# Performance work log

Hardware: AMD Instinct MI355X
Metric: run time of the kernel (lower is better)

## Reference

```python
import jax, jax.numpy as jnp
import numpy as np
import math

B, S, D, DFF = 32, 2048, 512, 512


def setup_inputs() -> dict:
    key = jax.random.key(0)
    ks = jax.random.split(key, 10)
    s = 1.0 / math.sqrt(D)
    inp = {
        "x": jax.random.normal(ks[0], (B, S, D), dtype=jnp.float32),
        "Wq": jax.random.uniform(ks[1], (DFF, D), jnp.float32, -s, s),
        "bq": jax.random.uniform(ks[2], (DFF,), jnp.float32, -s, s),
        "Wk": jax.random.uniform(ks[3], (DFF, D), jnp.float32, -s, s),
        "bk": jax.random.uniform(ks[4], (DFF,), jnp.float32, -s, s),
        "Wv": jax.random.uniform(ks[5], (DFF, D), jnp.float32, -s, s),
        "bv": jax.random.uniform(ks[6], (DFF,), jnp.float32, -s, s),
        "Wt": jax.random.uniform(ks[7], (1, S), jnp.float32, -1.0 / math.sqrt(S), 1.0 / math.sqrt(S)),
        "bt": jax.random.uniform(ks[8], (1,), jnp.float32, -1.0 / math.sqrt(S), 1.0 / math.sqrt(S)),
    }
    return inp


def reference(x, Wq, bq, Wk, bk, Wv, bv, Wt, bt):
    # QKV projections: [B,S,DFF]
    q = jnp.einsum('bsd,fd->bsf', x, Wq) + bq
    k = jnp.einsum('bsd,fd->bsf', x, Wk) + bk
    v = jnp.einsum('bsd,fd->bsf', x, Wv) + bv
    # attention scores: [B,S,S]
    scores = jnp.einsum('bsf,btf->bst', q, k) / math.sqrt(DFF)
    # temporal reduction Linear(S->1): [B,S,1] -> [B,S]
    ta = jnp.einsum('bst,t->bs', scores, Wt[0]) + bt[0]
    # V-weighted sum: [B,DFF]
    latent = jnp.einsum('bsf,bs->bf', v, ta)
    return latent
```

## Files before the change

kernel.cpp:

```cpp
#include <hip/hip_runtime.h>

#define NB 32
#define NS 2048
#define ND 512
#define NFF 512
#define SCALE 0.044194173824159216f
#define CPB 32
#define ROWS 64

__device__ __forceinline__ float dot4(float4 a, float4 b) {
    return a.x * b.x + a.y * b.y + a.z * b.z + a.w * b.w;
}

__device__ __forceinline__ float wave_reduce(float p) {
#pragma unroll
    for (int m = 1; m < 64; m <<= 1) p += __shfl_xor(p, m, 64);
    return p;
}

__global__ void __launch_bounds__(256) k_xw(const float* __restrict__ x,
                                            const float* __restrict__ Wt,
                                            float* __restrict__ xwp) {
    const int b = blockIdx.x >> 5;
    const int chunk = blockIdx.x & 31;
    const int s0 = chunk * ROWS;
    const int t = threadIdx.x;
    const int col = t & 127;
    const int half = t >> 7;

    const float4* xb = (const float4*)(x + (size_t)b * NS * ND);
    float4 acc = make_float4(0.f, 0.f, 0.f, 0.f);
#pragma unroll 8
    for (int i = 0; i < 32; i++) {
        int s = s0 + half + 2 * i;
        float w = Wt[s];
        float4 v = xb[(size_t)s * 128 + col];
        acc.x += w * v.x; acc.y += w * v.y; acc.z += w * v.z; acc.w += w * v.w;
    }
    __shared__ float4 red[128];
    if (half == 1) red[col] = acc;
    __syncthreads();
    if (half == 0) {
        float4 o = red[col];
        o.x += acc.x; o.y += acc.y; o.z += acc.z; o.w += acc.w;
        ((float4*)xwp)[(size_t)blockIdx.x * 128 + col] = o;
    }
}

__global__ void __launch_bounds__(1024, 1)
k_mid(const float* __restrict__ xwp, const float* __restrict__ Wt,
      const float* __restrict__ Wk, const float* __restrict__ bk,
      const float* __restrict__ Wq, const float* __restrict__ bq,
      const float* __restrict__ bt, float* __restrict__ wqs,
      float* __restrict__ cb2) {
    const int b = blockIdx.x;
    const int t = threadIdx.x;
    const int c4 = t & 127;
    const int grp = t >> 7;
    __shared__ __align__(16) float4 tmp4[1024];
    __shared__ __align__(16) float sxw[ND];
    __shared__ float skw[NFF];
    __shared__ float sW[16];
    __shared__ float ssw;

    {
        const float4* xp = (const float4*)(xwp + (size_t)b * CPB * ND) + c4;
        float4 a = make_float4(0.f, 0.f, 0.f, 0.f);
#pragma unroll
        for (int c = 0; c < 4; c++) {
            float4 v = xp[(size_t)(grp * 4 + c) * 128];
            a.x += v.x; a.y += v.y; a.z += v.z; a.w += v.w;
        }
        tmp4[t] = a;
    }
    if (t < 64) {
        float s = 0.f;
#pragma unroll
        for (int i = 0; i < 32; i++) s += Wt[t + 64 * i];
        s = wave_reduce(s);
        if (t == 0) ssw = s;
    }
    __syncthreads();
    if (t < 128) {
        float4 a = tmp4[t];
#pragma unroll
        for (int g = 1; g < 8; g++) {
            float4 v = tmp4[g * 128 + t];
            a.x += v.x; a.y += v.y; a.z += v.z; a.w += v.w;
        }
        ((float4*)sxw)[t] = a;
    }
    __syncthreads();

    const int wv = t >> 6;
    const int lane = t & 63;
    const float sw = ssw;
    const float4 xa = ((const float4*)sxw)[lane];
    const float4 xc = ((const float4*)sxw)[64 + lane];
    float cbp = 0.f;
#pragma unroll
    for (int j = 0; j < 4; j++) {
        const int f = wv * 32 + j * 8;
        float p[8];
#pragma unroll
        for (int u = 0; u < 8; u++) {
            const float4* r = (const float4*)(Wk + (size_t)(f + u) * ND);
            p[u] = dot4(xa, r[lane]) + dot4(xc, r[64 + lane]);
        }
#pragma unroll
        for (int m = 1; m < 64; m <<= 1) {
#pragma unroll
            for (int u = 0; u < 8; u++) p[u] += __shfl_xor(p[u], m, 64);
        }
        if (lane == 0) {
#pragma unroll
            for (int u = 0; u < 8; u++) {
                float k = SCALE * (p[u] + bk[f + u] * sw);
                skw[f + u] = k;
                cbp += k * bq[f + u];
            }
        }
    }
    if (lane == 0) sW[wv] = cbp;
    __syncthreads();

    {
        float4 acc = make_float4(0.f, 0.f, 0.f, 0.f);
        const float4* wq4 = (const float4*)Wq + c4;
#pragma unroll 4
        for (int j = 0; j < 64; j++) {
            int f = grp * 64 + j;
            float kf = skw[f];
            float4 v = wq4[(size_t)f * 128];
            acc.x += kf * v.x; acc.y += kf * v.y;
            acc.z += kf * v.z; acc.w += kf * v.w;
        }
        tmp4[t] = acc;
    }
    __syncthreads();
    if (t < 128) {
        float4 a = tmp4[t];
#pragma unroll
        for (int g = 1; g < 8; g++) {
            float4 v = tmp4[g * 128 + t];
            a.x += v.x; a.y += v.y; a.z += v.z; a.w += v.w;
        }
        ((float4*)(wqs + b * ND))[t] = a;
    }
    if (t == 0) {
        float cb = 0.f;
#pragma unroll
        for (int i = 0; i < 16; i++) cb += sW[i];
        cb2[b] = cb + bt[0];
    }
}

__global__ void __launch_bounds__(256) k_ta_xt(const float* __restrict__ x,
                                               const float* __restrict__ wqs,
                                               const float* __restrict__ cb2,
                                               float* __restrict__ xtp,
                                               float* __restrict__ stp) {
    const int b = blockIdx.x >> 5;
    const int chunk = blockIdx.x & 31;
    const int wv = threadIdx.x >> 6;
    const int lane = threadIdx.x & 63;
    const float4* xb = (const float4*)(x + (size_t)b * NS * ND);
    const float4* wq4 = (const float4*)(wqs + b * ND);
    const float4 w0 = wq4[lane];
    const float4 w1 = wq4[64 + lane];
    const float c = cb2[b];

    float4 a0 = make_float4(0.f, 0.f, 0.f, 0.f);
    float4 a1 = make_float4(0.f, 0.f, 0.f, 0.f);
    float sta = 0.f;
#pragma unroll
    for (int pass = 0; pass < 2; pass++) {
        const int sbase = chunk * ROWS + wv * 16 + pass * 8;
        float4 v0[8], v1[8];
        float pd[8];
#pragma unroll
        for (int i = 0; i < 8; i++) {
            int s = sbase + i;
            v0[i] = xb[(size_t)s * 128 + lane];
            v1[i] = xb[(size_t)s * 128 + 64 + lane];
            pd[i] = dot4(v0[i], w0) + dot4(v1[i], w1);
        }
#pragma unroll
        for (int m = 1; m < 64; m <<= 1) {
#pragma unroll
            for (int i = 0; i < 8; i++) pd[i] += __shfl_xor(pd[i], m, 64);
        }
#pragma unroll
        for (int i = 0; i < 8; i++) {
            float ta = pd[i] + c;
            a0.x += ta * v0[i].x; a0.y += ta * v0[i].y;
            a0.z += ta * v0[i].z; a0.w += ta * v0[i].w;
            a1.x += ta * v1[i].x; a1.y += ta * v1[i].y;
            a1.z += ta * v1[i].z; a1.w += ta * v1[i].w;
            sta += ta;
        }
    }
    __shared__ float4 sh0[4][64];
    __shared__ float4 sh1[4][64];
    __shared__ float sW[4];
    sh0[wv][lane] = a0;
    sh1[wv][lane] = a1;
    if (lane == 0) sW[wv] = sta;
    __syncthreads();
    const int t = threadIdx.x;
    float4* dst = (float4*)xtp + (size_t)blockIdx.x * 128;
    if (t < 64) {
        float4 s0 = sh0[0][t], s1 = sh0[1][t], s2 = sh0[2][t], s3 = sh0[3][t];
        dst[t] = make_float4(s0.x + s1.x + s2.x + s3.x,
                             s0.y + s1.y + s2.y + s3.y,
                             s0.z + s1.z + s2.z + s3.z,
                             s0.w + s1.w + s2.w + s3.w);
    } else if (t < 128) {
        int l = t - 64;
        float4 s0 = sh1[0][l], s1 = sh1[1][l], s2 = sh1[2][l], s3 = sh1[3][l];
        dst[64 + l] = make_float4(s0.x + s1.x + s2.x + s3.x,
                                  s0.y + s1.y + s2.y + s3.y,
                                  s0.z + s1.z + s2.z + s3.z,
                                  s0.w + s1.w + s2.w + s3.w);
    } else if (t == 128) {
        stp[blockIdx.x] = sW[0] + sW[1] + sW[2] + sW[3];
    }
}

__global__ void __launch_bounds__(1024, 1)
k_fin(const float* __restrict__ xtp, const float* __restrict__ stp,
      const float* __restrict__ Wv, const float* __restrict__ bv,
      float* __restrict__ out) {
    const int b = blockIdx.x;
    const int t = threadIdx.x;
    const int c4 = t & 127;
    const int grp = t >> 7;
    __shared__ __align__(16) float4 tmp4[1024];
    __shared__ __align__(16) float sxt[ND];
    __shared__ float sst;

    {
        const float4* xp = (const float4*)(xtp + (size_t)b * CPB * ND) + c4;
        float4 a = make_float4(0.f, 0.f, 0.f, 0.f);
#pragma unroll
        for (int c = 0; c < 4; c++) {
            float4 v = xp[(size_t)(grp * 4 + c) * 128];
            a.x += v.x; a.y += v.y; a.z += v.z; a.w += v.w;
        }
        tmp4[t] = a;
    }
    if (t < 64) {
        float s = (t < CPB) ? stp[b * CPB + t] : 0.f;
        s = wave_reduce(s);
        if (t == 0) sst = s;
    }
    __syncthreads();
    if (t < 128) {
        float4 a = tmp4[t];
#pragma unroll
        for (int g = 1; g < 8; g++) {
            float4 v = tmp4[g * 128 + t];
            a.x += v.x; a.y += v.y; a.z += v.z; a.w += v.w;
        }
        ((float4*)sxt)[t] = a;
    }
    __syncthreads();

    const int wv = t >> 6;
    const int lane = t & 63;
    const float4 xa = ((const float4*)sxt)[lane];
    const float4 xc = ((const float4*)sxt)[64 + lane];
    const float stb = sst;
#pragma unroll
    for (int j = 0; j < 4; j++) {
        const int f = wv * 32 + j * 8;
        float p[8];
#pragma unroll
        for (int u = 0; u < 8; u++) {
            const float4* r = (const float4*)(Wv + (size_t)(f + u) * ND);
            p[u] = dot4(xa, r[lane]) + dot4(xc, r[64 + lane]);
        }
#pragma unroll
        for (int m = 1; m < 64; m <<= 1) {
#pragma unroll
            for (int u = 0; u < 8; u++) p[u] += __shfl_xor(p[u], m, 64);
        }
        if (lane == 0) {
#pragma unroll
            for (int u = 0; u < 8; u++)
                out[b * NFF + f + u] = p[u] + bv[f + u] * stb;
        }
    }
}

extern "C" void kernel_launch(void* const* d_in, const int* in_sizes, int n_in,
                              void* d_out, int out_size, void* d_ws, size_t ws_size,
                              hipStream_t stream) {
    const float* x  = (const float*)d_in[0];
    const float* Wq = (const float*)d_in[1];
    const float* bq = (const float*)d_in[2];
    const float* Wk = (const float*)d_in[3];
    const float* bk = (const float*)d_in[4];
    const float* Wv = (const float*)d_in[5];
    const float* bv = (const float*)d_in[6];
    const float* Wt = (const float*)d_in[7];
    const float* bt = (const float*)d_in[8];
    float* out = (float*)d_out;

    float* w = (float*)d_ws;
    float* xwp = w;
    float* xtp = w + 524288;
    float* stp = w + 1048576;
    float* wqs = w + 1049600;
    float* cb2 = w + 1065984;

    k_xw<<<NB * CPB, 256, 0, stream>>>(x, Wt, xwp);
    k_mid<<<NB, 1024, 0, stream>>>(xwp, Wt, Wk, bk, Wq, bq, bt, wqs, cb2);
    k_ta_xt<<<NB * CPB, 256, 0, stream>>>(x, wqs, cb2, xtp, stp);
    k_fin<<<NB, 1024, 0, stream>>>(xtp, stp, Wv, bv, out);
}
```

Measured before the change: 276.9 us.

## Split k_mid and k_fin across eight feature-group blocks per batch

The two small per-batch kernels (k_mid, k_fin) previously ran only 32 blocks of 1024 threads. Each is now split into 8 blocks of 256 threads, each handling 64 output features, giving 256 blocks to fill more CUs. Each k_mid block writes a partial wqs vector and a partial cb2 term, and k_ta_xt sums the 8 partials when it loads them. The trade-off is redundant reduction of xwp/xtp in every group block and extra partial-sum reads in k_ta_xt.

```diff
diff --git a/kernel.cpp b/kernel.cpp
--- a/kernel.cpp
+++ b/kernel.cpp
@@ -47,28 +47,29 @@
     }
 }
 
-__global__ void __launch_bounds__(1024, 1)
+__global__ void __launch_bounds__(256)
 k_mid(const float* __restrict__ xwp, const float* __restrict__ Wt,
       const float* __restrict__ Wk, const float* __restrict__ bk,
       const float* __restrict__ Wq, const float* __restrict__ bq,
-      const float* __restrict__ bt, float* __restrict__ wqs,
-      float* __restrict__ cb2) {
-    const int b = blockIdx.x;
+      const float* __restrict__ bt, float* __restrict__ wqsp,
+      float* __restrict__ cb2p) {
+    const int b = blockIdx.x >> 3;
+    const int g = blockIdx.x & 7;
     const int t = threadIdx.x;
     const int c4 = t & 127;
-    const int grp = t >> 7;
-    __shared__ __align__(16) float4 tmp4[1024];
+    const int half = t >> 7;
+    __shared__ __align__(16) float4 tmp4[256];
     __shared__ __align__(16) float sxw[ND];
-    __shared__ float skw[NFF];
-    __shared__ float sW[16];
+    __shared__ float skw[64];
+    __shared__ float sW[4];
     __shared__ float ssw;
 
     {
         const float4* xp = (const float4*)(xwp + (size_t)b * CPB * ND) + c4;
         float4 a = make_float4(0.f, 0.f, 0.f, 0.f);
 #pragma unroll
-        for (int c = 0; c < 4; c++) {
-            float4 v = xp[(size_t)(grp * 4 + c) * 128];
+        for (int c = 0; c < 16; c++) {
+            float4 v = xp[(size_t)(half * 16 + c) * 128];
             a.x += v.x; a.y += v.y; a.z += v.z; a.w += v.w;
         }
         tmp4[t] = a;
@@ -82,12 +83,8 @@
     }
     __syncthreads();
     if (t < 128) {
-        float4 a = tmp4[t];
-#pragma unroll
-        for (int g = 1; g < 8; g++) {
-            float4 v = tmp4[g * 128 + t];
-            a.x += v.x; a.y += v.y; a.z += v.z; a.w += v.w;
-        }
+        float4 a = tmp4[t], v = tmp4[128 + t];
+        a.x += v.x; a.y += v.y; a.z += v.z; a.w += v.w;
         ((float4*)sxw)[t] = a;
     }
     __syncthreads();
@@ -97,10 +94,11 @@
     const float sw = ssw;
     const float4 xa = ((const float4*)sxw)[lane];
     const float4 xc = ((const float4*)sxw)[64 + lane];
+    const int fbase = g * 64;
     float cbp = 0.f;
 #pragma unroll
-    for (int j = 0; j < 4; j++) {
-        const int f = wv * 32 + j * 8;
+    for (int j = 0; j < 2; j++) {
+        const int f = fbase + wv * 16 + j * 8;
         float p[8];
 #pragma unroll
         for (int u = 0; u < 8; u++) {
@@ -116,7 +114,7 @@
 #pragma unroll
             for (int u = 0; u < 8; u++) {
                 float k = SCALE * (p[u] + bk[f + u] * sw);
-                skw[f + u] = k;
+                skw[wv * 16 + j * 8 + u] = k;
                 cbp += k * bq[f + u];
             }
         }
@@ -125,39 +123,27 @@
     __syncthreads();
 
     {
-        float4 acc = make_float4(0.f, 0.f, 0.f, 0.f);
-        const float4* wq4 = (const float4*)Wq + c4;
-#pragma unroll 4
+        const float* wp = Wq + (size_t)fbase * ND + t;
+        float a0 = 0.f, a1 = 0.f;
+#pragma unroll 8
         for (int j = 0; j < 64; j++) {
-            int f = grp * 64 + j;
-            float kf = skw[f];
-            float4 v = wq4[(size_t)f * 128];
-            acc.x += kf * v.x; acc.y += kf * v.y;
-            acc.z += kf * v.z; acc.w += kf * v.w;
-        }
-        tmp4[t] = acc;
-    }
-    __syncthreads();
-    if (t < 128) {
-        float4 a = tmp4[t];
-#pragma unroll
-        for (int g = 1; g < 8; g++) {
-            float4 v = tmp4[g * 128 + t];
-            a.x += v.x; a.y += v.y; a.z += v.z; a.w += v.w;
-        }
-        ((float4*)(wqs + b * ND))[t] = a;
+            float kf = skw[j];
+            a0 += kf * wp[(size_t)j * ND];
+            a1 += kf * wp[(size_t)j * ND + 256];
+        }
+        wqsp[(size_t)blockIdx.x * ND + t] = a0;
+        wqsp[(size_t)blockIdx.x * ND + 256 + t] = a1;
     }
     if (t == 0) {
-        float cb = 0.f;
-#pragma unroll
-        for (int i = 0; i < 16; i++) cb += sW[i];
-        cb2[b] = cb + bt[0];
+        float cb = sW[0] + sW[1] + sW[2] + sW[3];
+        if (g == 0) cb += bt[0];
+        cb2p[blockIdx.x] = cb;
     }
 }
 
 __global__ void __launch_bounds__(256) k_ta_xt(const float* __restrict__ x,
-                                               const float* __restrict__ wqs,
-                                               const float* __restrict__ cb2,
+                                               const float* __restrict__ wqsp,
+                                               const float* __restrict__ cb2p,
                                                float* __restrict__ xtp,
                                                float* __restrict__ stp) {
     const int b = blockIdx.x >> 5;
@@ -165,10 +151,19 @@
     const int wv = threadIdx.x >> 6;
     const int lane = threadIdx.x & 63;
     const float4* xb = (const float4*)(x + (size_t)b * NS * ND);
-    const float4* wq4 = (const float4*)(wqs + b * ND);
-    const float4 w0 = wq4[lane];
-    const float4 w1 = wq4[64 + lane];
-    const float c = cb2[b];
+
+    float4 w0 = make_float4(0.f, 0.f, 0.f, 0.f);
+    float4 w1 = make_float4(0.f, 0.f, 0.f, 0.f);
+    float c = 0.f;
+#pragma unroll
+    for (int gg = 0; gg < 8; gg++) {
+        const float4* wg = (const float4*)(wqsp + (size_t)(b * 8 + gg) * ND);
+        float4 u0 = wg[lane];
+        float4 u1 = wg[64 + lane];
+        w0.x += u0.x; w0.y += u0.y; w0.z += u0.z; w0.w += u0.w;
+        w1.x += u1.x; w1.y += u1.y; w1.z += u1.z; w1.w += u1.w;
+        c += cb2p[b * 8 + gg];
+    }
 
     float4 a0 = make_float4(0.f, 0.f, 0.f, 0.f);
     float4 a1 = make_float4(0.f, 0.f, 0.f, 0.f);
@@ -227,15 +222,16 @@
     }
 }
 
-__global__ void __launch_bounds__(1024, 1)
+__global__ void __launch_bounds__(256)
 k_fin(const float* __restrict__ xtp, const float* __restrict__ stp,
       const float* __restrict__ Wv, const float* __restrict__ bv,
       float* __restrict__ out) {
-    const int b = blockIdx.x;
+    const int b = blockIdx.x >> 3;
+    const int g = blockIdx.x & 7;
     const int t = threadIdx.x;
     const int c4 = t & 127;
-    const int grp = t >> 7;
-    __shared__ __align__(16) float4 tmp4[1024];
+    const int half = t >> 7;
+    __shared__ __align__(16) float4 tmp4[256];
     __shared__ __align__(16) float sxt[ND];
     __shared__ float sst;
 
@@ -243,8 +239,8 @@
         const float4* xp = (const float4*)(xtp + (size_t)b * CPB * ND) + c4;
         float4 a = make_float4(0.f, 0.f, 0.f, 0.f);
 #pragma unroll
-        for (int c = 0; c < 4; c++) {
-            float4 v = xp[(size_t)(grp * 4 + c) * 128];
+        for (int c = 0; c < 16; c++) {
+            float4 v = xp[(size_t)(half * 16 + c) * 128];
             a.x += v.x; a.y += v.y; a.z += v.z; a.w += v.w;
         }
         tmp4[t] = a;
@@ -256,12 +252,8 @@
     }
     __syncthreads();
     if (t < 128) {
-        float4 a = tmp4[t];
-#pragma unroll
-        for (int g = 1; g < 8; g++) {
-            float4 v = tmp4[g * 128 + t];
-            a.x += v.x; a.y += v.y; a.z += v.z; a.w += v.w;
-        }
+        float4 a = tmp4[t], v = tmp4[128 + t];
+        a.x += v.x; a.y += v.y; a.z += v.z; a.w += v.w;
         ((float4*)sxt)[t] = a;
     }
     __syncthreads();
@@ -272,8 +264,8 @@
     const float4 xc = ((const float4*)sxt)[64 + lane];
     const float stb = sst;
 #pragma unroll
-    for (int j = 0; j < 4; j++) {
-        const int f = wv * 32 + j * 8;
+    for (int j = 0; j < 2; j++) {
+        const int f = g * 64 + wv * 16 + j * 8;
         float p[8];
 #pragma unroll
         for (int u = 0; u < 8; u++) {
@@ -308,14 +300,14 @@
     float* out = (float*)d_out;
 
     float* w = (float*)d_ws;
-    float* xwp = w;
-    float* xtp = w + 524288;
-    float* stp = w + 1048576;
-    float* wqs = w + 1049600;
-    float* cb2 = w + 1065984;
+    float* xwp  = w;
+    float* xtp  = w + 524288;
+    float* stp  = w + 1048576;
+    float* wqsp = w + 1049600;
+    float* cb2p = w + 1180672;
 
     k_xw<<<NB * CPB, 256, 0, stream>>>(x, Wt, xwp);
-    k_mid<<<NB, 1024, 0, stream>>>(xwp, Wt, Wk, bk, Wq, bq, bt, wqs, cb2);
-    k_ta_xt<<<NB * CPB, 256, 0, stream>>>(x, wqs, cb2, xtp, stp);
-    k_fin<<<NB, 1024, 0, stream>>>(xtp, stp, Wv, bv, out);
-}
+    k_mid<<<NB * 8, 256, 0, stream>>>(xwp, Wt, Wk, bk, Wq, bq, bt, wqsp, cb2p);
+    k_ta_xt<<<NB * CPB, 256, 0, stream>>>(x, wqsp, cb2p, xtp, stp);
+    k_fin<<<NB * 8, 256, 0, stream>>>(xtp, stp, Wv, bv, out);
+}
```

Measured after the change: 252.3 us. -8.9%, faster.
